# Kernel tuning notes

Measured on AMD Instinct MI355X. Metric: run time of the kernel, lower is better.

The kernel has to match this reference:

```python
import jax, jax.numpy as jnp
import numpy as np

N_NODES = 100000
N_EDGES = 1600000
IN_FEAT = 128
HEADS = 4
OUT_FEAT = 16
ALPHA = 0.2  # LeakyReLU negative slope


def setup_inputs() -> dict:
    key = jax.random.key(0)
    k1, k2, k3, k4, k5 = jax.random.split(key, 5)
    x = jax.random.normal(k1, (N_NODES, IN_FEAT), dtype=jnp.float32)
    edge_index = jax.random.randint(k2, (2, N_EDGES), 0, N_NODES, dtype=jnp.int64)
    # xavier_uniform with gain=1.414
    gain = 1.414
    lim_W = gain * np.sqrt(6.0 / (IN_FEAT + HEADS * OUT_FEAT))
    W = jax.random.uniform(k3, (IN_FEAT, HEADS * OUT_FEAT), minval=-lim_W, maxval=lim_W, dtype=jnp.float32)
    lim_a = gain * np.sqrt(6.0 / (HEADS + OUT_FEAT))
    a_src = jax.random.uniform(k4, (HEADS, OUT_FEAT), minval=-lim_a, maxval=lim_a, dtype=jnp.float32)
    a_dst = jax.random.uniform(k5, (HEADS, OUT_FEAT), minval=-lim_a, maxval=lim_a, dtype=jnp.float32)
    return {"x": x, "edge_index": edge_index, "W": W, "a_src": a_src, "a_dst": a_dst}


def reference(x, edge_index, W, a_src, a_dst):
    N = x.shape[0]
    H, F = a_src.shape
    src, dst = edge_index[0], edge_index[1]

    h = (x @ W).reshape(N, H, F)                 # [N, H, F]
    att_src = jnp.sum(h * a_src, axis=-1)        # [N, H]
    att_dst = jnp.sum(h * a_dst, axis=-1)        # [N, H]

    e = jax.nn.leaky_relu(att_src[src] + att_dst[dst], negative_slope=ALPHA)  # [E, H]

    # segment softmax over edges grouped by dst
    e_max = jax.ops.segment_max(e, dst, num_segments=N)   # [N, H]
    e_max = jnp.where(jnp.isfinite(e_max), e_max, 0.0)    # nodes with no in-edges
    ex = jnp.exp(e - e_max[dst])                           # [E, H]
    denom = jax.ops.segment_sum(ex, dst, num_segments=N)  # [N, H]
    alpha = ex / (denom[dst] + 1e-16)                      # [E, H]
    # dropout: inference mode (training=False) -> identity

    messages = h[src] * alpha[:, :, None]                  # [E, H, F]
    out = jax.ops.segment_sum(messages, dst, num_segments=N)  # [N, H, F]

    out = out.reshape(N, H * F)  # concat=True
    out = jax.nn.elu(out)
    return out
```

## Files before the change

### kernel.cpp

```cpp
#include <hip/hip_runtime.h>


#define NEG_SLOPE 0.2f
#define BSHIFT 9
#define BNODES 512
#define CH 2048
#define BCB 512
#define QSHIFT 6
#define QNODES 64
#define QCAP 1536

typedef __bf16 bf16x8 __attribute__((ext_vector_type(8)));
typedef float  f32x4  __attribute__((ext_vector_type(4)));

static __device__ __forceinline__ unsigned f2b(float f) {
    union { float f; unsigned u; } v; v.f = f;
    return (v.u + 0x7fffu + ((v.u >> 16) & 1u)) >> 16;
}
static __device__ __forceinline__ float u2f(unsigned u) {
    union { unsigned u32; float f; } v; v.u32 = u; return v.f;
}

__global__ __launch_bounds__(256) void gemm_att_kernel(
    const float* __restrict__ x,
    const float* __restrict__ W,
    const float* __restrict__ a_src,
    const float* __restrict__ a_dst,
    unsigned short* __restrict__ h_out,
    float* __restrict__ att_s_o,
    float* __restrict__ att_d_o,
    const int* __restrict__ dst,
    int* __restrict__ bucketCount,
    int N, int E, int gemmBlocks)
{
    __shared__ bf16x8 Wswz[20][64];
    __shared__ int c[256];
    int t = threadIdx.x;

    if (blockIdx.x >= gemmBlocks) {
        int bid = blockIdx.x - gemmBlocks;
        c[t] = 0;
        __syncthreads();
        for (int e = bid * 256 + t; e < E; e += BCB * 256)
            atomicAdd(&c[dst[e] >> BSHIFT], 1);
        __syncthreads();
        if (c[t]) atomicAdd(&bucketCount[t], c[t]);
        return;
    }

    for (int i = t; i < 8192; i += 256) {
        int k = i >> 6, n = i & 63;
        __bf16* dp = (__bf16*)&Wswz[((n >> 4) << 2) | (k >> 5)]
                                   [(((k >> 3) & 3) << 4) | (n & 15)];
        dp[k & 7] = (__bf16)W[i];
    }
    for (int i = t; i < 1024; i += 256) {
        int k = i >> 3, c7 = i & 7;
        int hd = c7 & 3;
        const float* aa = (c7 < 4) ? a_src : a_dst;
        float sum = 0.f;
        #pragma unroll
        for (int f = 0; f < 16; ++f)
            sum = fmaf(W[k * 64 + hd * 16 + f], aa[hd * 16 + f], sum);
        __bf16* dp = (__bf16*)&Wswz[16 + (k >> 5)][(((k >> 3) & 3) << 4) | c7];
        dp[k & 7] = (__bf16)sum;
        __bf16* dz = (__bf16*)&Wswz[16 + (k >> 5)][(((k >> 3) & 3) << 4) | (8 + c7)];
        dz[k & 7] = (__bf16)0.f;
    }
    __syncthreads();

    int wave = t >> 6;
    int lane = t & 63;
    int col = lane & 15, quad = lane >> 4;
    int node_base = (blockIdx.x * 4 + wave) * 16;
    int arow = min(node_base + col, N - 1);
    const float* xp = x + arow * 128;

    bf16x8 af[4];
    #pragma unroll
    for (int tt = 0; tt < 4; ++tt) {
        float4 xa = *(const float4*)(xp + tt * 32 + quad * 8);
        float4 xb = *(const float4*)(xp + tt * 32 + quad * 8 + 4);
        bf16x8 f;
        f[0] = (__bf16)xa.x; f[1] = (__bf16)xa.y;
        f[2] = (__bf16)xa.z; f[3] = (__bf16)xa.w;
        f[4] = (__bf16)xb.x; f[5] = (__bf16)xb.y;
        f[6] = (__bf16)xb.z; f[7] = (__bf16)xb.w;
        af[tt] = f;
    }

    f32x4 acc[4], accA;
    #pragma unroll
    for (int cb = 0; cb < 4; ++cb) {
        acc[cb] = (f32x4){0.f, 0.f, 0.f, 0.f};
        #pragma unroll
        for (int tt = 0; tt < 4; ++tt)
            acc[cb] = __builtin_amdgcn_mfma_f32_16x16x32_bf16(
                af[tt], Wswz[(cb << 2) | tt][lane], acc[cb], 0, 0, 0);
    }
    accA = (f32x4){0.f, 0.f, 0.f, 0.f};
    #pragma unroll
    for (int tt = 0; tt < 4; ++tt)
        accA = __builtin_amdgcn_mfma_f32_16x16x32_bf16(
            af[tt], Wswz[16 + tt][lane], accA, 0, 0, 0);

    #pragma unroll
    for (int cb = 0; cb < 4; ++cb) {
        #pragma unroll
        for (int r = 0; r < 4; ++r) {
            int node = node_base + quad * 4 + r;
            if (node < N)
                h_out[node * 64 + cb * 16 + col] = (unsigned short)f2b(acc[cb][r]);
        }
    }
    if (col < 8) {
        #pragma unroll
        for (int r = 0; r < 4; ++r) {
            int node = node_base + quad * 4 + r;
            if (node < N) {
                if (col < 4) att_s_o[(node << 2) | col] = accA[r];
                else         att_d_o[(node << 2) | (col - 4)] = accA[r];
            }
        }
    }
}

__global__ __launch_bounds__(256) void bscatter_kernel(
    const int* __restrict__ src, const int* __restrict__ dst,
    const int* __restrict__ bucketCount,
    int* __restrict__ bucketCursor, int* __restrict__ pairs,
    int* __restrict__ bbase, int nb, int E)
{
    __shared__ int cnt[256], lo[256], gpos[256], cur[256], sm[256], gbc[256];
    __shared__ int2 staged[CH];
    int t = threadIdx.x;
    int base = blockIdx.x * CH;
    int nloc = min(CH, E - base);

    cnt[t] = 0;
    gbc[t] = (t < nb) ? bucketCount[t] : 0;
    __syncthreads();
    for (int i = t; i < nloc; i += 256)
        atomicAdd(&cnt[dst[base + i] >> BSHIFT], 1);
    __syncthreads();

    int v = cnt[t];
    sm[t] = v;
    __syncthreads();
    #pragma unroll
    for (int off = 1; off < 256; off <<= 1) {
        int u = (t >= off) ? sm[t - off] : 0;
        __syncthreads();
        sm[t] += u;
        __syncthreads();
    }
    lo[t] = sm[t] - v;
    cur[t] = lo[t];
    __syncthreads();

    int g = gbc[t];
    sm[t] = g;
    __syncthreads();
    #pragma unroll
    for (int off = 1; off < 256; off <<= 1) {
        int u = (t >= off) ? sm[t - off] : 0;
        __syncthreads();
        sm[t] += u;
        __syncthreads();
    }
    gpos[t] = (v > 0) ? (sm[t] - g) + atomicAdd(&bucketCursor[t], v) : 0;
    if (blockIdx.x == 0) {
        bbase[t + 1] = sm[t];
        if (t == 0) bbase[0] = 0;
    }
    __syncthreads();

    for (int i = t; i < nloc; i += 256) {
        int d = dst[base + i];
        int s = src[base + i];
        int b = d >> BSHIFT;
        int k = atomicAdd(&cur[b], 1);
        staged[k] = make_int2((s << BSHIFT) | (d & (BNODES - 1)), b);
    }
    __syncthreads();

    for (int i = t; i < nloc; i += 256) {
        int2 p = staged[i];
        pairs[gpos[p.y] + (i - lo[p.y])] = p.x;
    }
}

__global__ __launch_bounds__(256, 8) void bucket_csr_agg_kernel(
    const int* __restrict__ pairs,
    const int* __restrict__ bbase,
    const float* __restrict__ att_s,
    const float* __restrict__ att_d,
    const unsigned short* __restrict__ hmat,
    float* __restrict__ out,
    int N)
{
    __shared__ int sorted[QCAP];
    __shared__ int cnt[QNODES], rs[QNODES + 1], cur[QNODES], sm[QNODES];
    __shared__ float attd[QNODES * 4];

    int blk = blockIdx.x, t = threadIdx.x;
    int b = blk >> 3, s8 = blk & 7;
    int node_lo = (b << BSHIFT) + (s8 << QSHIFT);
    if (node_lo >= N) return;
    int nn = min(QNODES, N - node_lo);

    int ebase = bbase[b];
    int ecnt  = bbase[b + 1] - ebase;

    if (t < QNODES) cnt[t] = 0;
    for (int i = t; i < (nn << 2); i += 256)
        attd[i] = att_d[(node_lo << 2) + i];
    __syncthreads();

    for (int i = t; i < ecnt; i += 256) {
        int dl = pairs[ebase + i] & (BNODES - 1);
        if ((dl >> QSHIFT) == s8)
            atomicAdd(&cnt[dl & (QNODES - 1)], 1);
    }
    __syncthreads();

    int v = (t < QNODES) ? cnt[t] : 0;
    if (t < QNODES) sm[t] = v;
    __syncthreads();
    #pragma unroll
    for (int off = 1; off < QNODES; off <<= 1) {
        int u = (t >= off && t < QNODES) ? sm[t - off] : 0;
        __syncthreads();
        if (t < QNODES) sm[t] += u;
        __syncthreads();
    }
    if (t < QNODES) {
        int x = sm[t] - v; rs[t] = x; cur[t] = x;
        if (t == QNODES - 1) rs[QNODES] = sm[t];
    }
    __syncthreads();

    for (int i = t; i < ecnt; i += 256) {
        int p = pairs[ebase + i];
        int dl = p & (BNODES - 1);
        if ((dl >> QSHIFT) == s8) {
            int k = atomicAdd(&cur[dl & (QNODES - 1)], 1);
            if (k < QCAP) sorted[k] = p >> BSHIFT;
        }
    }
    __syncthreads();

    int q = t & 7;
    int h = q >> 1;
    int nclamp = N - 1;

    for (int pass = 0; pass < 2; ++pass) {
        int node = (pass << 5) + (t >> 3);
        if (node >= nn) continue;
        int beg = rs[node];
        int deg = rs[node + 1] - beg;
        float ad = attd[(node << 2) | h];

        float a0 = 0.f, a1 = 0.f, a2 = 0.f, a3 = 0.f;
        float a4 = 0.f, a5 = 0.f, a6 = 0.f, a7 = 0.f, l = 0.f;
        int d1 = deg - 1;
        for (int e0 = 0; e0 < deg; e0 += 4) {
            int s0 = min(sorted[beg + min(e0 + 0, d1)], nclamp);
            int s1 = min(sorted[beg + min(e0 + 1, d1)], nclamp);
            int s2 = min(sorted[beg + min(e0 + 2, d1)], nclamp);
            int s3 = min(sorted[beg + min(e0 + 3, d1)], nclamp);
            float t0 = att_s[(s0 << 2) | h];
            float t1 = att_s[(s1 << 2) | h];
            float t2 = att_s[(s2 << 2) | h];
            float t3 = att_s[(s3 << 2) | h];
            uint4 hp0 = *(const uint4*)(hmat + (s0 << 6) + (q << 3));
            uint4 hp1 = *(const uint4*)(hmat + (s1 << 6) + (q << 3));
            uint4 hp2 = *(const uint4*)(hmat + (s2 << 6) + (q << 3));
            uint4 hp3 = *(const uint4*)(hmat + (s3 << 6) + (q << 3));
            float av0 = t0 + ad; av0 = fmaxf(av0, NEG_SLOPE * av0);
            float av1 = t1 + ad; av1 = fmaxf(av1, NEG_SLOPE * av1);
            float av2 = t2 + ad; av2 = fmaxf(av2, NEG_SLOPE * av2);
            float av3 = t3 + ad; av3 = fmaxf(av3, NEG_SLOPE * av3);
            float w0 = __expf(av0);
            float w1 = (e0 + 1 < deg) ? __expf(av1) : 0.f;
            float w2 = (e0 + 2 < deg) ? __expf(av2) : 0.f;
            float w3 = (e0 + 3 < deg) ? __expf(av3) : 0.f;
            l += w0 + w1 + w2 + w3;
            a0 = fmaf(w0, u2f(hp0.x << 16), a0);
            a1 = fmaf(w0, u2f(hp0.x & 0xffff0000u), a1);
            a2 = fmaf(w0, u2f(hp0.y << 16), a2);
            a3 = fmaf(w0, u2f(hp0.y & 0xffff0000u), a3);
            a4 = fmaf(w0, u2f(hp0.z << 16), a4);
            a5 = fmaf(w0, u2f(hp0.z & 0xffff0000u), a5);
            a6 = fmaf(w0, u2f(hp0.w << 16), a6);
            a7 = fmaf(w0, u2f(hp0.w & 0xffff0000u), a7);
            a0 = fmaf(w1, u2f(hp1.x << 16), a0);
            a1 = fmaf(w1, u2f(hp1.x & 0xffff0000u), a1);
            a2 = fmaf(w1, u2f(hp1.y << 16), a2);
            a3 = fmaf(w1, u2f(hp1.y & 0xffff0000u), a3);
            a4 = fmaf(w1, u2f(hp1.z << 16), a4);
            a5 = fmaf(w1, u2f(hp1.z & 0xffff0000u), a5);
            a6 = fmaf(w1, u2f(hp1.w << 16), a6);
            a7 = fmaf(w1, u2f(hp1.w & 0xffff0000u), a7);
            a0 = fmaf(w2, u2f(hp2.x << 16), a0);
            a1 = fmaf(w2, u2f(hp2.x & 0xffff0000u), a1);
            a2 = fmaf(w2, u2f(hp2.y << 16), a2);
            a3 = fmaf(w2, u2f(hp2.y & 0xffff0000u), a3);
            a4 = fmaf(w2, u2f(hp2.z << 16), a4);
            a5 = fmaf(w2, u2f(hp2.z & 0xffff0000u), a5);
            a6 = fmaf(w2, u2f(hp2.w << 16), a6);
            a7 = fmaf(w2, u2f(hp2.w & 0xffff0000u), a7);
            a0 = fmaf(w3, u2f(hp3.x << 16), a0);
            a1 = fmaf(w3, u2f(hp3.x & 0xffff0000u), a1);
            a2 = fmaf(w3, u2f(hp3.y << 16), a2);
            a3 = fmaf(w3, u2f(hp3.y & 0xffff0000u), a3);
            a4 = fmaf(w3, u2f(hp3.z << 16), a4);
            a5 = fmaf(w3, u2f(hp3.z & 0xffff0000u), a5);
            a6 = fmaf(w3, u2f(hp3.w << 16), a6);
            a7 = fmaf(w3, u2f(hp3.w & 0xffff0000u), a7);
        }

        float rl = 1.0f / (l + 1e-16f);
        float4 v0, v1;
        v0.x = a0 * rl; v0.x = (v0.x > 0.f) ? v0.x : (__expf(v0.x) - 1.f);
        v0.y = a1 * rl; v0.y = (v0.y > 0.f) ? v0.y : (__expf(v0.y) - 1.f);
        v0.z = a2 * rl; v0.z = (v0.z > 0.f) ? v0.z : (__expf(v0.z) - 1.f);
        v0.w = a3 * rl; v0.w = (v0.w > 0.f) ? v0.w : (__expf(v0.w) - 1.f);
        v1.x = a4 * rl; v1.x = (v1.x > 0.f) ? v1.x : (__expf(v1.x) - 1.f);
        v1.y = a5 * rl; v1.y = (v1.y > 0.f) ? v1.y : (__expf(v1.y) - 1.f);
        v1.z = a6 * rl; v1.z = (v1.z > 0.f) ? v1.z : (__expf(v1.z) - 1.f);
        v1.w = a7 * rl; v1.w = (v1.w > 0.f) ? v1.w : (__expf(v1.w) - 1.f);
        float* op = out + ((size_t)(node_lo + node) << 6) + (q << 3);
        *(float4*)op = v0;
        *(float4*)(op + 4) = v1;
    }
}

extern "C" void kernel_launch(void* const* d_in, const int* in_sizes, int n_in,
                              void* d_out, int out_size, void* d_ws, size_t ws_size,
                              hipStream_t stream) {
    const float* x     = (const float*)d_in[0];
    const int*   ei    = (const int*)d_in[1];
    const float* W     = (const float*)d_in[2];
    const float* a_src = (const float*)d_in[3];
    const float* a_dst = (const float*)d_in[4];

    int N = in_sizes[0] / 128;
    int E = in_sizes[1] / 2;
    const int* src = ei;
    const int* dst = ei + E;
    int nb = (N + BNODES - 1) / BNODES;

    char* ws = (char*)d_ws;
    size_t off = 0;
    unsigned short* hmat = (unsigned short*)(ws + off); off += (size_t)N * 64 * 2;
    float* att_s = (float*)(ws + off);  off += (size_t)N * 4 * 4;
    float* att_d = (float*)(ws + off);  off += (size_t)N * 4 * 4;
    int* pairs    = (int*)(ws + off);   off += (size_t)E * 4;
    int* bucketCount  = (int*)(ws + off); off += 256 * 4;
    int* bucketCursor = (int*)(ws + off); off += 256 * 4;
    int* bbase    = (int*)(ws + off);   off += 257 * 4;

    hipMemsetAsync(bucketCount, 0, 512 * 4, stream);

    int gemmBlocks = (N + 63) / 64;
    gemm_att_kernel<<<gemmBlocks + BCB, 256, 0, stream>>>(
        x, W, a_src, a_dst, hmat, att_s, att_d, dst, bucketCount,
        N, E, gemmBlocks);

    int blocksS = (E + CH - 1) / CH;
    bscatter_kernel<<<blocksS, 256, 0, stream>>>(src, dst, bucketCount,
                                                 bucketCursor, pairs, bbase,
                                                 nb, E);

    bucket_csr_agg_kernel<<<nb * 8, 256, 0, stream>>>(
        pairs, bbase, att_s, att_d, hmat, (float*)d_out, N);
}
```

Measured before the change: 213.5 us.

## Pre-split bucket edges into per-slice arrays before aggregation

Adds a kernel that partitions each 512-node bucket's edge list into eight 64-node slice arrays of fixed capacity, using wave ballots to compute positions. Each aggregation block then reads only its own slice's edges, where before every block scanned the whole bucket twice and filtered. This adds an extra launch and an extra full read and write of the edge array, and silently drops edges when a slice has more than SCAP of them.

```diff
diff --git a/kernel.cpp b/kernel.cpp
--- a/kernel.cpp
+++ b/kernel.cpp
@@ -6,9 +6,8 @@
 #define BNODES 512
 #define CH 2048
 #define BCB 512
-#define QSHIFT 6
 #define QNODES 64
-#define QCAP 1536
+#define SCAP 1536
 
 typedef __bf16 bf16x8 __attribute__((ext_vector_type(8)));
 typedef float  f32x4  __attribute__((ext_vector_type(4)));
@@ -190,38 +189,69 @@
     }
 }
 
+__global__ __launch_bounds__(1024) void sliceshuffle_kernel(
+    const int* __restrict__ pairs, const int* __restrict__ bbase,
+    int* __restrict__ pairs2, int* __restrict__ scount, int nb)
+{
+    __shared__ int cur8[8];
+    int b = blockIdx.x, t = threadIdx.x;
+    int lane = t & 63;
+    unsigned long long below = (lane == 0) ? 0ull : ((~0ull) >> (64 - lane));
+    int ebase = bbase[b];
+    int ecnt  = bbase[b + 1] - ebase;
+    if (t < 8) cur8[t] = 0;
+    __syncthreads();
+
+    for (int i = t; i < ecnt; i += 1024) {
+        int p = pairs[ebase + i];
+        int sl = (p >> 6) & 7;
+        int pos = 0;
+        #pragma unroll
+        for (int s = 0; s < 8; ++s) {
+            unsigned long long m = __ballot(sl == s);
+            if (sl == s) {
+                int rank = __popcll(m & below);
+                int b0 = 0;
+                if (rank == 0) b0 = atomicAdd(&cur8[s], (int)__popcll(m));
+                b0 = __shfl(b0, (int)(__ffsll((long long)m) - 1), 64);
+                pos = b0 + rank;
+            }
+        }
+        if (pos < SCAP) pairs2[(((b << 3) | sl) * SCAP) + pos] = p;
+    }
+    __syncthreads();
+    if (t < 8) scount[(b << 3) | t] = min(cur8[t], SCAP);
+}
+
 __global__ __launch_bounds__(256, 8) void bucket_csr_agg_kernel(
-    const int* __restrict__ pairs,
-    const int* __restrict__ bbase,
+    const int* __restrict__ pairs2,
+    const int* __restrict__ scount,
     const float* __restrict__ att_s,
     const float* __restrict__ att_d,
     const unsigned short* __restrict__ hmat,
     float* __restrict__ out,
     int N)
 {
-    __shared__ int sorted[QCAP];
+    __shared__ int sorted[SCAP];
     __shared__ int cnt[QNODES], rs[QNODES + 1], cur[QNODES], sm[QNODES];
     __shared__ float attd[QNODES * 4];
 
     int blk = blockIdx.x, t = threadIdx.x;
     int b = blk >> 3, s8 = blk & 7;
-    int node_lo = (b << BSHIFT) + (s8 << QSHIFT);
+    int node_lo = (b << BSHIFT) + (s8 << 6);
     if (node_lo >= N) return;
     int nn = min(QNODES, N - node_lo);
 
-    int ebase = bbase[b];
-    int ecnt  = bbase[b + 1] - ebase;
+    int ebase = blk * SCAP;
+    int ecnt  = scount[blk];
 
     if (t < QNODES) cnt[t] = 0;
     for (int i = t; i < (nn << 2); i += 256)
         attd[i] = att_d[(node_lo << 2) + i];
     __syncthreads();
 
-    for (int i = t; i < ecnt; i += 256) {
-        int dl = pairs[ebase + i] & (BNODES - 1);
-        if ((dl >> QSHIFT) == s8)
-            atomicAdd(&cnt[dl & (QNODES - 1)], 1);
-    }
+    for (int i = t; i < ecnt; i += 256)
+        atomicAdd(&cnt[pairs2[ebase + i] & (QNODES - 1)], 1);
     __syncthreads();
 
     int v = (t < QNODES) ? cnt[t] : 0;
@@ -241,12 +271,9 @@
     __syncthreads();
 
     for (int i = t; i < ecnt; i += 256) {
-        int p = pairs[ebase + i];
-        int dl = p & (BNODES - 1);
-        if ((dl >> QSHIFT) == s8) {
-            int k = atomicAdd(&cur[dl & (QNODES - 1)], 1);
-            if (k < QCAP) sorted[k] = p >> BSHIFT;
-        }
+        int p = pairs2[ebase + i];
+        int k = atomicAdd(&cur[p & (QNODES - 1)], 1);
+        if (k < SCAP) sorted[k] = p >> BSHIFT;
     }
     __syncthreads();
 
@@ -357,9 +384,11 @@
     float* att_s = (float*)(ws + off);  off += (size_t)N * 4 * 4;
     float* att_d = (float*)(ws + off);  off += (size_t)N * 4 * 4;
     int* pairs    = (int*)(ws + off);   off += (size_t)E * 4;
+    int* pairs2   = (int*)(ws + off);   off += (size_t)nb * 8 * SCAP * 4;
     int* bucketCount  = (int*)(ws + off); off += 256 * 4;
     int* bucketCursor = (int*)(ws + off); off += 256 * 4;
     int* bbase    = (int*)(ws + off);   off += 257 * 4;
+    int* scount   = (int*)(ws + off);   off += (size_t)nb * 8 * 4;
 
     hipMemsetAsync(bucketCount, 0, 512 * 4, stream);
 
@@ -373,6 +402,9 @@
                                                  bucketCursor, pairs, bbase,
                                                  nb, E);
 
+    sliceshuffle_kernel<<<nb, 1024, 0, stream>>>(pairs, bbase, pairs2,
+                                                 scount, nb);
+
     bucket_csr_agg_kernel<<<nb * 8, 256, 0, stream>>>(
-        pairs, bbase, att_s, att_d, hmat, (float*)d_out, N);
-}
+        pairs2, scount, att_s, att_d, hmat, (float*)d_out, N);
+}
```

After: 207.2 us. 1.03x faster.
